# Kernel tuning notes

Measured on AMD Instinct MI355X. Metric: run time of the kernel, lower is better.

Reference implementation:

```python
import jax, jax.numpy as jnp
import numpy as np


def setup_inputs() -> dict:
    key = jax.random.key(0)
    k1, k2, k3 = jax.random.split(key, 3)
    b, n, h, d = 2, 2048, 16, 64
    q = jax.random.normal(k1, (b, n, h, d), dtype=jnp.float32)
    k = jax.random.normal(k2, (b, n, h, d), dtype=jnp.float32)
    v = jax.random.normal(k3, (b, n, h, d), dtype=jnp.float32)
    return {"q": q, "k": k, "v": v, "is_causal": 1}


def reference(q, k, v, is_causal):
    # q, k, v: [b, n, h, d] -> attention computed in [b, h, n, d] layout
    b, n, h, d = q.shape
    scale = 1.0 / jnp.sqrt(jnp.asarray(d, dtype=q.dtype))
    # scores: [b, h, n_q, n_k]
    scores = jnp.einsum("bqhd,bkhd->bhqk", q, k) * scale
    if is_causal:
        causal_mask = jnp.triu(jnp.ones((n, n), dtype=bool), k=1)  # True above diag
        scores = jnp.where(causal_mask[None, None], -jnp.inf, scores)
    attn = jax.nn.softmax(scores, axis=-1)
    out = jnp.einsum("bhqk,bkhd->bqhd", attn, v)  # back to [b, n, h, d]
    return out
```

## Files before the change

kernel.cpp:

```cpp
#include <hip/hip_runtime.h>
#include <hip/hip_bf16.h>

namespace {

constexpr int Nn = 2048;
constexpr int Hh = 16;
constexpr int Dd = 64;
constexpr int ROWSTR = Hh * Dd;
constexpr int KVB = 64;
constexpr int NTILES = Nn / KVB;
constexpr size_t IMG_TILE = 16384;
constexpr size_t WS_NEED = (size_t)32 * NTILES * IMG_TILE;

typedef __bf16 bf16x8 __attribute__((ext_vector_type(8)));
typedef __bf16 bf16x4 __attribute__((ext_vector_type(4)));
typedef float  f32x16 __attribute__((ext_vector_type(16)));

constexpr float MSHIFT = 16.0f;

__device__ __forceinline__ void gload_lds16(const char* g, char* l) {
  __builtin_amdgcn_global_load_lds(
      (const __attribute__((address_space(1))) void*)g,
      (__attribute__((address_space(3))) void*)l, 16, 0, 0);
}
__device__ __forceinline__ void drain_vmcnt0() {
  asm volatile("s_waitcnt vmcnt(0)" ::: "memory");
}

__global__ __launch_bounds__(256, 2) void prep_kernel(
    const float* __restrict__ Kg, const float* __restrict__ Vg,
    char* __restrict__ ws) {
  const int bid = blockIdx.x;
  const int bh  = bid & 31;
  const int T   = bid >> 5;
  const int tid = threadIdx.x;
  const int b = bh >> 4, h = bh & 15;
  const size_t base = ((size_t)b * Nn * Hh + h) * Dd;
  const float* kp = Kg + base;
  const float* vp = Vg + base;
  char* img = ws + (size_t)(bh * NTILES + T) * IMG_TILE;

  {
    const int row = tid >> 2;
    const int seg = tid & 3;
    const float* kr = kp + (size_t)(T * 64 + row) * ROWSTR + seg * 16;
    float4 f0 = ((const float4*)kr)[0];
    float4 f1 = ((const float4*)kr)[1];
    float4 f2 = ((const float4*)kr)[2];
    float4 f3 = ((const float4*)kr)[3];
    const int half = row >> 5, l31r = row & 31;
    char* slotp = img + (half * 4 + seg) * 1024;
    bf16x8 w0 = { (__bf16)f0.x, (__bf16)f0.y, (__bf16)f0.z, (__bf16)f0.w,
                  (__bf16)f1.x, (__bf16)f1.y, (__bf16)f1.z, (__bf16)f1.w };
    bf16x8 w1 = { (__bf16)f2.x, (__bf16)f2.y, (__bf16)f2.z, (__bf16)f2.w,
                  (__bf16)f3.x, (__bf16)f3.y, (__bf16)f3.z, (__bf16)f3.w };
    *(bf16x8*)(slotp + l31r * 16) = w0;
    *(bf16x8*)(slotp + (l31r + 32) * 16) = w1;
  }
  char* imgV = img + 8192;
#pragma unroll
  for (int e2 = 0; e2 < 2; ++e2) {
    const int e = e2 * 256 + tid;
    const int slotV = e >> 6, lane = e & 63;
    const int kc = slotV >> 1, df = slotV & 1;
    const int l31e = lane & 31, g2e = lane >> 5;
    const int d = 32 * df + l31e;
    const size_t kv0 = (size_t)(T * 64 + 16 * kc + 4 * g2e);
    const float* vb = vp + d;
    bf16x8 w;
#pragma unroll
    for (int i2 = 0; i2 < 4; ++i2) w[i2]     = (__bf16)vb[(kv0 + i2) * ROWSTR];
#pragma unroll
    for (int i2 = 0; i2 < 4; ++i2) w[4 + i2] = (__bf16)vb[(kv0 + 8 + i2) * ROWSTR];
    *(bf16x8*)(imgV + slotV * 1024 + lane * 16) = w;
  }
}

__global__ __launch_bounds__(256, 2) void fattn_kernel(
    const float* __restrict__ Qg, const char* __restrict__ ws,
    const int* __restrict__ flag, float* __restrict__ Og) {
  __shared__ __align__(16) char smem[2][2][16384];

  const int tid  = threadIdx.x;
  const int lane = tid & 63;
  const int wv   = tid >> 6;
  const int grp  = wv >> 1;
  const int st   = wv & 1;
  const int l31  = lane & 31;
  const int g2   = lane >> 5;

  const int bid = blockIdx.x;
  const int bh  = ((bid & 7) << 2) | ((bid >> 3) & 3);
  const int j   = bid >> 5;
  const int b   = bh >> 4;
  const int h   = bh & 15;
  const int causal = flag[0];

  const size_t base = ((size_t)b * Nn * Hh + h) * Dd;
  const float* qp = Qg + base;
  const char*  img = ws + (size_t)bh * NTILES * IMG_TILE;
  float*       op = Og + base;

  const float SCALE = 0.125f * 1.44269504088896340736f;

  bf16x8 vone;
#pragma unroll
  for (int e = 0; e < 8; ++e) vone[e] = (__bf16)1.0f;

  for (int pass = 0; pass < 2; ++pass) {
    const int Tq = pass ? j : (31 - j);
    const int qs = Tq * 64 + st * 32;
    const int NI = causal ? ((Tq + 2) >> 1) : (NTILES / 2);
    const int nC = causal ? ((Tq >= grp) ? (((Tq - grp) >> 1) + 1) : 0)
                          : (NTILES / 2);

    __syncthreads();

    bf16x8 qf[4];
#pragma unroll
    for (int dc = 0; dc < 4; ++dc) {
      const float* qrow = qp + (size_t)(qs + l31) * ROWSTR + dc * 16 + g2 * 8;
      float4 a = *(const float4*)qrow;
      float4 c = *(const float4*)(qrow + 4);
      qf[dc][0] = (__bf16)(a.x * SCALE); qf[dc][1] = (__bf16)(a.y * SCALE);
      qf[dc][2] = (__bf16)(a.z * SCALE); qf[dc][3] = (__bf16)(a.w * SCALE);
      qf[dc][4] = (__bf16)(c.x * SCALE); qf[dc][5] = (__bf16)(c.y * SCALE);
      qf[dc][6] = (__bf16)(c.z * SCALE); qf[dc][7] = (__bf16)(c.w * SCALE);
    }

    f32x16 acc0 = {};
    f32x16 acc1 = {};
    f32x16 accl = {};

#pragma unroll
    for (int it = 0; it < 8; ++it)
      gload_lds16(img + (it * 256 + tid) * 16,
                  &smem[0][0][0] + (it * 256 + tid) * 16);
    __builtin_amdgcn_sched_barrier(0);

    for (int i = 0; i < NI; ++i) {
      drain_vmcnt0();
      __syncthreads();
      const bool pf = (i + 1 < NI);
      if (pf) {
        const char* src = img + (size_t)(2 * i + 2) * IMG_TILE;
        char* dst = &smem[(i + 1) & 1][0][0];
#pragma unroll
        for (int it = 0; it < 8; ++it)
          gload_lds16(src + (it * 256 + tid) * 16, dst + (it * 256 + tid) * 16);
        __builtin_amdgcn_sched_barrier(0);
      }

      if (i < nC) {
        const char* kb = &smem[i & 1][grp][0];
        const char* vb = kb + 8192;

        f32x16 s0, s1;
#pragma unroll
        for (int rr = 0; rr < 16; ++rr) { s0[rr] = -MSHIFT; s1[rr] = -MSHIFT; }
        __builtin_amdgcn_s_setprio(1);
#pragma unroll
        for (int dc = 0; dc < 4; ++dc) {
          bf16x8 kf0 = *(const bf16x8*)(kb + (dc)     * 1024 + lane * 16);
          bf16x8 kf1 = *(const bf16x8*)(kb + (4 + dc) * 1024 + lane * 16);
          s0 = __builtin_amdgcn_mfma_f32_32x32x16_bf16(kf0, qf[dc], s0, 0, 0, 0);
          s1 = __builtin_amdgcn_mfma_f32_32x32x16_bf16(kf1, qf[dc], s1, 0, 0, 0);
        }
        __builtin_amdgcn_s_setprio(0);

        if (causal && (2 * i + grp) == Tq) {
          const int kvb = Tq * KVB;
          const int qrow = qs + l31;
#pragma unroll
          for (int rr = 0; rr < 16; ++rr) {
            int rm = (rr & 3) + ((rr >> 2) << 3) + (g2 << 2);
            if (kvb + rm > qrow)      s0[rr] = -INFINITY;
            if (kvb + 32 + rm > qrow) s1[rr] = -INFINITY;
          }
        }

#pragma unroll
        for (int rr = 0; rr < 16; ++rr) {
          s0[rr] = __builtin_amdgcn_exp2f(s0[rr]);
          s1[rr] = __builtin_amdgcn_exp2f(s1[rr]);
        }

        bf16x8 pa[4];
#pragma unroll
        for (int kc = 0; kc < 4; ++kc) {
          const f32x16& sv = (kc < 2) ? s0 : s1;
          const int rbase = (kc & 1) * 8;
#pragma unroll
          for (int jj = 0; jj < 8; ++jj) pa[kc][jj] = (__bf16)sv[rbase + jj];
        }

        __builtin_amdgcn_s_setprio(1);
#pragma unroll
        for (int kc = 0; kc < 4; ++kc) {
          bf16x8 vf0 = *(const bf16x8*)(vb + (kc * 2)     * 1024 + lane * 16);
          bf16x8 vf1 = *(const bf16x8*)(vb + (kc * 2 + 1) * 1024 + lane * 16);
          acc0 = __builtin_amdgcn_mfma_f32_32x32x16_bf16(pa[kc], vf0, acc0, 0, 0, 0);
          acc1 = __builtin_amdgcn_mfma_f32_32x32x16_bf16(pa[kc], vf1, acc1, 0, 0, 0);
          accl = __builtin_amdgcn_mfma_f32_32x32x16_bf16(pa[kc], vone, accl, 0, 0, 0);
        }
        __builtin_amdgcn_s_setprio(0);
      }
    }

    drain_vmcnt0();
    __syncthreads();
    float* arena = (float*)&smem[1][0][0];
    if (grp == 1) {
      float* ab = arena + st * 2112;
#pragma unroll
      for (int rr = 0; rr < 16; ++rr) {
        int rm = (rr & 3) + ((rr >> 2) << 3) + (g2 << 2);
        ab[rm * 64 + l31]      = acc0[rr];
        ab[rm * 64 + 32 + l31] = acc1[rr];
        ab[2048 + rm]          = accl[rr];
      }
    }
    __syncthreads();
    if (grp == 0) {
      const float* ab = arena + st * 2112;
#pragma unroll
      for (int rr = 0; rr < 16; ++rr) {
        const int rm = (rr & 3) + ((rr >> 2) << 3) + (g2 << 2);
        const float lT = accl[rr] + ab[2048 + rm];
        const float li = 1.0f / lT;
        const float o0 = (acc0[rr] + ab[rm * 64 + l31])      * li;
        const float o1 = (acc1[rr] + ab[rm * 64 + 32 + l31]) * li;
        const size_t row = (size_t)(qs + rm) * ROWSTR;
        op[row + l31]      = o0;
        op[row + 32 + l31] = o1;
      }
    }
  }
}

__device__ __forceinline__ int swzK(int row, int colByte) {
  return (row * 128 + colByte) ^ ((row & 7) << 4);
}
__device__ __forceinline__ int swzV(int row, int colByte) {
  return (row * 128 + colByte) ^ (((row & 7) << 4) | (((row >> 3) & 1) << 3));
}
struct SR { float4 k[4]; float v[16]; };
__device__ __forceinline__ void fb_issue(const float* kp, const float* vp,
                                         int kv0, int tid, SR& s) {
#pragma unroll
  for (int it = 0; it < 4; ++it) {
    int idx = it * 256 + tid;
    int kvr = idx >> 4, c4 = idx & 15;
    s.k[it] = *(const float4*)(kp + (size_t)(kv0 + kvr) * ROWSTR + c4 * 4);
  }
#pragma unroll
  for (int it = 0; it < 4; ++it) {
    int idx = it * 256 + tid;
    int d8 = idx & 63, kv4 = idx >> 6;
#pragma unroll
    for (int i2 = 0; i2 < 4; ++i2)
      s.v[it * 4 + i2] = vp[(size_t)(kv0 + kv4 * 4 + i2) * ROWSTR + d8];
  }
}
__device__ __forceinline__ void fb_write(char* kb, char* vb, int tid, const SR& s) {
#pragma unroll
  for (int it = 0; it < 4; ++it) {
    int idx = it * 256 + tid;
    int kvr = idx >> 4, c4 = idx & 15;
    bf16x4 w = { (__bf16)s.k[it].x, (__bf16)s.k[it].y,
                 (__bf16)s.k[it].z, (__bf16)s.k[it].w };
    *(bf16x4*)(kb + swzK(kvr, c4 * 8)) = w;
  }
#pragma unroll
  for (int it = 0; it < 4; ++it) {
    int idx = it * 256 + tid;
    int d8 = idx & 63, kv4 = idx >> 6;
    bf16x4 w = { (__bf16)s.v[it * 4 + 0], (__bf16)s.v[it * 4 + 1],
                 (__bf16)s.v[it * 4 + 2], (__bf16)s.v[it * 4 + 3] };
    *(bf16x4*)(vb + swzV(d8, kv4 * 8)) = w;
  }
}
__global__ __launch_bounds__(256, 2) void fattn_fb(
    const float* __restrict__ Qg, const float* __restrict__ Kg,
    const float* __restrict__ Vg, const int* __restrict__ flag,
    float* __restrict__ Og) {
  __shared__ char smem[16384];
  const int tid  = threadIdx.x;
  const int lane = tid & 63;
  const int wv   = tid >> 6;
  const int l31  = lane & 31;
  const int g2   = lane >> 5;
  const int bid = blockIdx.x;
  const int pidx = bid >> 1;
  const int side = bid & 1;
  const int bh  = ((pidx & 7) << 2) | (pidx >> 6);
  const int ti  = (pidx >> 3) & 7;
  const int b   = bh >> 4;
  const int h   = bh & 15;
  const int causal = flag[0];
  const int Tq  = side ? ti : (15 - ti);
  const size_t base = ((size_t)b * Nn * Hh + h) * Dd;
  const float* qp = Qg + base;
  const float* kp = Kg + base;
  const float* vp = Vg + base;
  float*       op = Og + base;
  const float SCALE = 0.125f * 1.44269504088896340736f;
  const int qs = Tq * 128 + wv * 32;
  const int Tblock = causal ? (2 * Tq + 2) : NTILES;
  const int Twave  = causal ? ((qs + 31) / KVB + 1) : NTILES;
  bf16x8 qf[4];
#pragma unroll
  for (int dc = 0; dc < 4; ++dc) {
    const float* qrow = qp + (size_t)(qs + l31) * ROWSTR + dc * 16 + g2 * 8;
    float4 a = *(const float4*)qrow;
    float4 c = *(const float4*)(qrow + 4);
    qf[dc][0] = (__bf16)(a.x * SCALE); qf[dc][1] = (__bf16)(a.y * SCALE);
    qf[dc][2] = (__bf16)(a.z * SCALE); qf[dc][3] = (__bf16)(a.w * SCALE);
    qf[dc][4] = (__bf16)(c.x * SCALE); qf[dc][5] = (__bf16)(c.y * SCALE);
    qf[dc][6] = (__bf16)(c.z * SCALE); qf[dc][7] = (__bf16)(c.w * SCALE);
  }
  f32x16 acc0 = {}, acc1 = {};
  float m_run = -INFINITY, l_run = 0.0f;
  SR st;
  fb_issue(kp, vp, 0, tid, st);
  fb_write(smem, smem + 8192, tid, st);
  for (int t = 0; t < Tblock; ++t) {
    __syncthreads();
    const bool pf = (t + 1 < Tblock);
    if (pf) fb_issue(kp, vp, (t + 1) * KVB, tid, st);
    if (t < Twave) {
      const char* kb = smem;
      const char* vb = smem + 8192;
      f32x16 s0 = {}, s1 = {};
#pragma unroll
      for (int dc = 0; dc < 4; ++dc) {
        bf16x8 kf0 = *(const bf16x8*)(kb + swzK(l31,      32 * dc + 16 * g2));
        bf16x8 kf1 = *(const bf16x8*)(kb + swzK(32 + l31, 32 * dc + 16 * g2));
        s0 = __builtin_amdgcn_mfma_f32_32x32x16_bf16(kf0, qf[dc], s0, 0, 0, 0);
        s1 = __builtin_amdgcn_mfma_f32_32x32x16_bf16(kf1, qf[dc], s1, 0, 0, 0);
      }
      if (causal && t == Twave - 1) {
        const int kvb = t * KVB;
        const int qrow = qs + l31;
#pragma unroll
        for (int rr = 0; rr < 16; ++rr) {
          int rm = (rr & 3) + ((rr >> 2) << 3) + (g2 << 2);
          if (kvb + rm > qrow)      s0[rr] = -INFINITY;
          if (kvb + 32 + rm > qrow) s1[rr] = -INFINITY;
        }
      }
      float p8[8];
#pragma unroll
      for (int e = 0; e < 8; ++e)
        p8[e] = fmaxf(fmaxf(s0[e], s0[e + 8]), fmaxf(s1[e], s1[e + 8]));
      float mt = fmaxf(fmaxf(fmaxf(p8[0], p8[1]), fmaxf(p8[2], p8[3])),
                       fmaxf(fmaxf(p8[4], p8[5]), fmaxf(p8[6], p8[7])));
      mt = fmaxf(mt, __shfl_xor(mt, 32));
      const float mnew = fmaxf(m_run, mt);
#pragma unroll
      for (int rr = 0; rr < 16; ++rr) {
        s0[rr] = __builtin_amdgcn_exp2f(s0[rr] - mnew);
        s1[rr] = __builtin_amdgcn_exp2f(s1[rr] - mnew);
      }
      float q8[8];
#pragma unroll
      for (int e = 0; e < 8; ++e)
        q8[e] = (s0[e] + s0[e + 8]) + (s1[e] + s1[e + 8]);
      float rs = ((q8[0] + q8[1]) + (q8[2] + q8[3])) +
                 ((q8[4] + q8[5]) + (q8[6] + q8[7]));
      rs += __shfl_xor(rs, 32);
      if (__all(mt <= m_run)) {
        l_run += rs;
      } else {
        const float alpha = __builtin_amdgcn_exp2f(m_run - mnew);
#pragma unroll
        for (int rr = 0; rr < 16; ++rr) {
          float at = __shfl(alpha, (rr & 3) + ((rr >> 2) << 3) + (g2 << 2));
          acc0[rr] *= at;
          acc1[rr] *= at;
        }
        l_run = l_run * alpha + rs;
        m_run = mnew;
      }
      bf16x8 pa[4];
#pragma unroll
      for (int kc = 0; kc < 4; ++kc) {
        const f32x16& sv = (kc < 2) ? s0 : s1;
        const int rbase = (kc & 1) * 8;
#pragma unroll
        for (int jj = 0; jj < 8; ++jj) pa[kc][jj] = (__bf16)sv[rbase + jj];
      }
#pragma unroll
      for (int kc = 0; kc < 4; ++kc) {
        const int cb = 32 * kc + 8 * g2;
#pragma unroll
        for (int df = 0; df < 2; ++df) {
          const int row = 32 * df + l31;
          bf16x4 v0 = *(const bf16x4*)(vb + swzV(row, cb));
          bf16x4 v1 = *(const bf16x4*)(vb + swzV(row, cb + 16));
          bf16x8 vf = __builtin_shufflevector(v0, v1, 0, 1, 2, 3, 4, 5, 6, 7);
          if (df == 0)
            acc0 = __builtin_amdgcn_mfma_f32_32x32x16_bf16(pa[kc], vf, acc0, 0, 0, 0);
          else
            acc1 = __builtin_amdgcn_mfma_f32_32x32x16_bf16(pa[kc], vf, acc1, 0, 0, 0);
        }
      }
    }
    __syncthreads();
    if (pf) fb_write(smem, smem + 8192, tid, st);
  }
  const float linv = 1.0f / l_run;
#pragma unroll
  for (int rr = 0; rr < 16; ++rr) {
    const int rm = (rr & 3) + ((rr >> 2) << 3) + (g2 << 2);
    const float li = __shfl(linv, rm);
    const size_t row = (size_t)(qs + rm) * ROWSTR;
    op[row + l31]      = acc0[rr] * li;
    op[row + 32 + l31] = acc1[rr] * li;
  }
}

}

extern "C" void kernel_launch(void* const* d_in, const int* in_sizes, int n_in,
                              void* d_out, int out_size, void* d_ws, size_t ws_size,
                              hipStream_t stream) {
  (void)in_sizes; (void)n_in; (void)out_size;
  const float* q = (const float*)d_in[0];
  const float* k = (const float*)d_in[1];
  const float* v = (const float*)d_in[2];
  const int* flag = (const int*)d_in[3];
  float* out = (float*)d_out;
  if (ws_size >= WS_NEED) {
    char* ws = (char*)d_ws;
    prep_kernel<<<dim3(1024), dim3(256), 0, stream>>>(k, v, ws);
    fattn_kernel<<<dim3(512), dim3(256), 0, stream>>>(q, ws, flag, out);
  } else {
    fattn_fb<<<dim3(512), dim3(256), 0, stream>>>(q, k, v, flag, out);
  }
}
```

Baseline: 44.57 us.

## Split attention into 32-row query tiles with 4-way per-wave KV split

Query tiles shrink from 64 to 32 rows and each of the four waves now takes every fourth 32-key KV tile with its own double-buffered LDS region. Each wave runs its own pipeline with no block-wide barrier per iteration, and the grid doubles to 1024 blocks. At the end, three waves' partial results are reduced through LDS into wave 0. The aim is finer causal load balance, more parallelism and no per-tile syncs, at the cost of more Q reloads, a larger cross-wave reduction, and fewer MFMAs per loaded tile.

```diff
diff --git a/kernel.cpp b/kernel.cpp
--- a/kernel.cpp
+++ b/kernel.cpp
@@ -7,10 +7,10 @@
 constexpr int Hh = 16;
 constexpr int Dd = 64;
 constexpr int ROWSTR = Hh * Dd;
-constexpr int KVB = 64;
-constexpr int NTILES = Nn / KVB;
-constexpr size_t IMG_TILE = 16384;
-constexpr size_t WS_NEED = (size_t)32 * NTILES * IMG_TILE;
+constexpr int KVB = 32;
+constexpr int NT32 = Nn / KVB;
+constexpr size_t IMG_TILE = 8192;
+constexpr size_t WS_NEED = (size_t)32 * NT32 * IMG_TILE;
 
 typedef __bf16 bf16x8 __attribute__((ext_vector_type(8)));
 typedef __bf16 bf16x4 __attribute__((ext_vector_type(4)));
@@ -32,24 +32,24 @@
     char* __restrict__ ws) {
   const int bid = blockIdx.x;
   const int bh  = bid & 31;
-  const int T   = bid >> 5;
+  const int m   = bid >> 5;
   const int tid = threadIdx.x;
   const int b = bh >> 4, h = bh & 15;
   const size_t base = ((size_t)b * Nn * Hh + h) * Dd;
   const float* kp = Kg + base;
   const float* vp = Vg + base;
-  char* img = ws + (size_t)(bh * NTILES + T) * IMG_TILE;
+  char* img0 = ws + (size_t)(bh * NT32 + 2 * m) * IMG_TILE;
 
   {
     const int row = tid >> 2;
     const int seg = tid & 3;
-    const float* kr = kp + (size_t)(T * 64 + row) * ROWSTR + seg * 16;
+    const float* kr = kp + (size_t)(m * 64 + row) * ROWSTR + seg * 16;
     float4 f0 = ((const float4*)kr)[0];
     float4 f1 = ((const float4*)kr)[1];
     float4 f2 = ((const float4*)kr)[2];
     float4 f3 = ((const float4*)kr)[3];
-    const int half = row >> 5, l31r = row & 31;
-    char* slotp = img + (half * 4 + seg) * 1024;
+    char* slotp = img0 + (row >> 5) * IMG_TILE + seg * 1024;
+    const int l31r = row & 31;
     bf16x8 w0 = { (__bf16)f0.x, (__bf16)f0.y, (__bf16)f0.z, (__bf16)f0.w,
                   (__bf16)f1.x, (__bf16)f1.y, (__bf16)f1.z, (__bf16)f1.w };
     bf16x8 w1 = { (__bf16)f2.x, (__bf16)f2.y, (__bf16)f2.z, (__bf16)f2.w,
@@ -57,35 +57,35 @@
     *(bf16x8*)(slotp + l31r * 16) = w0;
     *(bf16x8*)(slotp + (l31r + 32) * 16) = w1;
   }
-  char* imgV = img + 8192;
 #pragma unroll
   for (int e2 = 0; e2 < 2; ++e2) {
     const int e = e2 * 256 + tid;
-    const int slotV = e >> 6, lane = e & 63;
-    const int kc = slotV >> 1, df = slotV & 1;
+    const int im = e >> 8;
+    const int r  = e & 255;
+    const int slotV = r >> 6;
+    const int lane  = r & 63;
+    const int kc2 = slotV >> 1, df = slotV & 1;
     const int l31e = lane & 31, g2e = lane >> 5;
     const int d = 32 * df + l31e;
-    const size_t kv0 = (size_t)(T * 64 + 16 * kc + 4 * g2e);
+    const size_t kv0 = (size_t)(m * 64 + im * 32 + 16 * kc2 + 4 * g2e);
     const float* vb = vp + d;
     bf16x8 w;
 #pragma unroll
     for (int i2 = 0; i2 < 4; ++i2) w[i2]     = (__bf16)vb[(kv0 + i2) * ROWSTR];
 #pragma unroll
     for (int i2 = 0; i2 < 4; ++i2) w[4 + i2] = (__bf16)vb[(kv0 + 8 + i2) * ROWSTR];
-    *(bf16x8*)(imgV + slotV * 1024 + lane * 16) = w;
+    *(bf16x8*)(img0 + im * IMG_TILE + 4096 + slotV * 1024 + lane * 16) = w;
   }
 }
 
 __global__ __launch_bounds__(256, 2) void fattn_kernel(
     const float* __restrict__ Qg, const char* __restrict__ ws,
     const int* __restrict__ flag, float* __restrict__ Og) {
-  __shared__ __align__(16) char smem[2][2][16384];
+  __shared__ __align__(16) char smem[4][2][8192];
 
   const int tid  = threadIdx.x;
   const int lane = tid & 63;
   const int wv   = tid >> 6;
-  const int grp  = wv >> 1;
-  const int st   = wv & 1;
   const int l31  = lane & 31;
   const int g2   = lane >> 5;
 
@@ -98,7 +98,7 @@
 
   const size_t base = ((size_t)b * Nn * Hh + h) * Dd;
   const float* qp = Qg + base;
-  const char*  img = ws + (size_t)bh * NTILES * IMG_TILE;
+  const char*  img = ws + (size_t)bh * NT32 * IMG_TILE;
   float*       op = Og + base;
 
   const float SCALE = 0.125f * 1.44269504088896340736f;
@@ -107,12 +107,14 @@
 #pragma unroll
   for (int e = 0; e < 8; ++e) vone[e] = (__bf16)1.0f;
 
+  char* buf0 = &smem[wv][0][0];
+  char* buf1 = &smem[wv][1][0];
+
   for (int pass = 0; pass < 2; ++pass) {
-    const int Tq = pass ? j : (31 - j);
-    const int qs = Tq * 64 + st * 32;
-    const int NI = causal ? ((Tq + 2) >> 1) : (NTILES / 2);
-    const int nC = causal ? ((Tq >= grp) ? (((Tq - grp) >> 1) + 1) : 0)
-                          : (NTILES / 2);
+    const int Tq = pass ? j : (63 - j);
+    const int qs = Tq * 32;
+    const int TL = causal ? Tq : (NT32 - 1);
+    const int nC = (TL >= wv) ? (((TL - wv) >> 2) + 1) : 0;
 
     __syncthreads();
 
@@ -132,86 +134,75 @@
     f32x16 acc1 = {};
     f32x16 accl = {};
 
-#pragma unroll
-    for (int it = 0; it < 8; ++it)
-      gload_lds16(img + (it * 256 + tid) * 16,
-                  &smem[0][0][0] + (it * 256 + tid) * 16);
-    __builtin_amdgcn_sched_barrier(0);
-
-    for (int i = 0; i < NI; ++i) {
+    if (nC > 0) {
+      const char* src = img + (size_t)wv * IMG_TILE;
+#pragma unroll
+      for (int it = 0; it < 8; ++it)
+        gload_lds16(src + it * 1024 + lane * 16, buf0 + it * 1024 + lane * 16);
+    }
+
+    for (int i = 0; i < nC; ++i) {
+      const int t = wv + 4 * i;
       drain_vmcnt0();
-      __syncthreads();
-      const bool pf = (i + 1 < NI);
-      if (pf) {
-        const char* src = img + (size_t)(2 * i + 2) * IMG_TILE;
-        char* dst = &smem[(i + 1) & 1][0][0];
+      __builtin_amdgcn_sched_barrier(0);
+      if (i + 1 < nC) {
+        const char* src = img + (size_t)(t + 4) * IMG_TILE;
+        char* dst = (i & 1) ? buf0 : buf1;
 #pragma unroll
         for (int it = 0; it < 8; ++it)
-          gload_lds16(src + (it * 256 + tid) * 16, dst + (it * 256 + tid) * 16);
+          gload_lds16(src + it * 1024 + lane * 16, dst + it * 1024 + lane * 16);
         __builtin_amdgcn_sched_barrier(0);
       }
-
-      if (i < nC) {
-        const char* kb = &smem[i & 1][grp][0];
-        const char* vb = kb + 8192;
-
-        f32x16 s0, s1;
-#pragma unroll
-        for (int rr = 0; rr < 16; ++rr) { s0[rr] = -MSHIFT; s1[rr] = -MSHIFT; }
-        __builtin_amdgcn_s_setprio(1);
-#pragma unroll
-        for (int dc = 0; dc < 4; ++dc) {
-          bf16x8 kf0 = *(const bf16x8*)(kb + (dc)     * 1024 + lane * 16);
-          bf16x8 kf1 = *(const bf16x8*)(kb + (4 + dc) * 1024 + lane * 16);
-          s0 = __builtin_amdgcn_mfma_f32_32x32x16_bf16(kf0, qf[dc], s0, 0, 0, 0);
-          s1 = __builtin_amdgcn_mfma_f32_32x32x16_bf16(kf1, qf[dc], s1, 0, 0, 0);
+      const char* kb = (i & 1) ? buf1 : buf0;
+      const char* vb = kb + 4096;
+
+      f32x16 s0;
+#pragma unroll
+      for (int rr = 0; rr < 16; ++rr) s0[rr] = -MSHIFT;
+      __builtin_amdgcn_s_setprio(1);
+#pragma unroll
+      for (int dc = 0; dc < 4; ++dc) {
+        bf16x8 kf = *(const bf16x8*)(kb + dc * 1024 + lane * 16);
+        s0 = __builtin_amdgcn_mfma_f32_32x32x16_bf16(kf, qf[dc], s0, 0, 0, 0);
+      }
+      __builtin_amdgcn_s_setprio(0);
+
+      if (causal && t == TL) {
+        const int kvb = t * KVB;
+        const int qrow = qs + l31;
+#pragma unroll
+        for (int rr = 0; rr < 16; ++rr) {
+          int rm = (rr & 3) + ((rr >> 2) << 3) + (g2 << 2);
+          if (kvb + rm > qrow) s0[rr] = -INFINITY;
         }
-        __builtin_amdgcn_s_setprio(0);
-
-        if (causal && (2 * i + grp) == Tq) {
-          const int kvb = Tq * KVB;
-          const int qrow = qs + l31;
-#pragma unroll
-          for (int rr = 0; rr < 16; ++rr) {
-            int rm = (rr & 3) + ((rr >> 2) << 3) + (g2 << 2);
-            if (kvb + rm > qrow)      s0[rr] = -INFINITY;
-            if (kvb + 32 + rm > qrow) s1[rr] = -INFINITY;
-          }
-        }
-
-#pragma unroll
-        for (int rr = 0; rr < 16; ++rr) {
-          s0[rr] = __builtin_amdgcn_exp2f(s0[rr]);
-          s1[rr] = __builtin_amdgcn_exp2f(s1[rr]);
-        }
-
-        bf16x8 pa[4];
-#pragma unroll
-        for (int kc = 0; kc < 4; ++kc) {
-          const f32x16& sv = (kc < 2) ? s0 : s1;
-          const int rbase = (kc & 1) * 8;
-#pragma unroll
-          for (int jj = 0; jj < 8; ++jj) pa[kc][jj] = (__bf16)sv[rbase + jj];
-        }
-
-        __builtin_amdgcn_s_setprio(1);
-#pragma unroll
-        for (int kc = 0; kc < 4; ++kc) {
-          bf16x8 vf0 = *(const bf16x8*)(vb + (kc * 2)     * 1024 + lane * 16);
-          bf16x8 vf1 = *(const bf16x8*)(vb + (kc * 2 + 1) * 1024 + lane * 16);
-          acc0 = __builtin_amdgcn_mfma_f32_32x32x16_bf16(pa[kc], vf0, acc0, 0, 0, 0);
-          acc1 = __builtin_amdgcn_mfma_f32_32x32x16_bf16(pa[kc], vf1, acc1, 0, 0, 0);
-          accl = __builtin_amdgcn_mfma_f32_32x32x16_bf16(pa[kc], vone, accl, 0, 0, 0);
-        }
-        __builtin_amdgcn_s_setprio(0);
-      }
-    }
-
-    drain_vmcnt0();
-    __syncthreads();
-    float* arena = (float*)&smem[1][0][0];
-    if (grp == 1) {
-      float* ab = arena + st * 2112;
+      }
+
+#pragma unroll
+      for (int rr = 0; rr < 16; ++rr) s0[rr] = __builtin_amdgcn_exp2f(s0[rr]);
+
+      bf16x8 pa0, pa1;
+#pragma unroll
+      for (int jj = 0; jj < 8; ++jj) { pa0[jj] = (__bf16)s0[jj];
+                                       pa1[jj] = (__bf16)s0[8 + jj]; }
+
+      __builtin_amdgcn_s_setprio(1);
+      {
+        bf16x8 v00 = *(const bf16x8*)(vb + 0 * 1024 + lane * 16);
+        bf16x8 v01 = *(const bf16x8*)(vb + 1 * 1024 + lane * 16);
+        bf16x8 v10 = *(const bf16x8*)(vb + 2 * 1024 + lane * 16);
+        bf16x8 v11 = *(const bf16x8*)(vb + 3 * 1024 + lane * 16);
+        acc0 = __builtin_amdgcn_mfma_f32_32x32x16_bf16(pa0, v00, acc0, 0, 0, 0);
+        acc1 = __builtin_amdgcn_mfma_f32_32x32x16_bf16(pa0, v01, acc1, 0, 0, 0);
+        accl = __builtin_amdgcn_mfma_f32_32x32x16_bf16(pa0, vone, accl, 0, 0, 0);
+        acc0 = __builtin_amdgcn_mfma_f32_32x32x16_bf16(pa1, v10, acc0, 0, 0, 0);
+        acc1 = __builtin_amdgcn_mfma_f32_32x32x16_bf16(pa1, v11, acc1, 0, 0, 0);
+        accl = __builtin_amdgcn_mfma_f32_32x32x16_bf16(pa1, vone, accl, 0, 0, 0);
+      }
+      __builtin_amdgcn_s_setprio(0);
+    }
+
+    if (wv != 0) {
+      float* ab = (float*)&smem[wv][0][0];
 #pragma unroll
       for (int rr = 0; rr < 16; ++rr) {
         int rm = (rr & 3) + ((rr >> 2) << 3) + (g2 << 2);
@@ -221,15 +212,19 @@
       }
     }
     __syncthreads();
-    if (grp == 0) {
-      const float* ab = arena + st * 2112;
+    if (wv == 0) {
+      const float* a1 = (const float*)&smem[1][0][0];
+      const float* a2 = (const float*)&smem[2][0][0];
+      const float* a3 = (const float*)&smem[3][0][0];
 #pragma unroll
       for (int rr = 0; rr < 16; ++rr) {
         const int rm = (rr & 3) + ((rr >> 2) << 3) + (g2 << 2);
-        const float lT = accl[rr] + ab[2048 + rm];
+        const float lT = accl[rr] + a1[2048 + rm] + a2[2048 + rm] + a3[2048 + rm];
         const float li = 1.0f / lT;
-        const float o0 = (acc0[rr] + ab[rm * 64 + l31])      * li;
-        const float o1 = (acc1[rr] + ab[rm * 64 + 32 + l31]) * li;
+        const float o0 = (acc0[rr] + a1[rm * 64 + l31] +
+                          a2[rm * 64 + l31] + a3[rm * 64 + l31]) * li;
+        const float o1 = (acc1[rr] + a1[rm * 64 + 32 + l31] +
+                          a2[rm * 64 + 32 + l31] + a3[rm * 64 + 32 + l31]) * li;
         const size_t row = (size_t)(qs + rm) * ROWSTR;
         op[row + l31]      = o0;
         op[row + 32 + l31] = o1;
@@ -306,8 +301,8 @@
   float*       op = Og + base;
   const float SCALE = 0.125f * 1.44269504088896340736f;
   const int qs = Tq * 128 + wv * 32;
-  const int Tblock = causal ? (2 * Tq + 2) : NTILES;
-  const int Twave  = causal ? ((qs + 31) / KVB + 1) : NTILES;
+  const int Tblock = causal ? (2 * Tq + 2) : 32;
+  const int Twave  = causal ? ((qs + 31) / 64 + 1) : 32;
   bf16x8 qf[4];
 #pragma unroll
   for (int dc = 0; dc < 4; ++dc) {
@@ -327,7 +322,7 @@
   for (int t = 0; t < Tblock; ++t) {
     __syncthreads();
     const bool pf = (t + 1 < Tblock);
-    if (pf) fb_issue(kp, vp, (t + 1) * KVB, tid, st);
+    if (pf) fb_issue(kp, vp, (t + 1) * 64, tid, st);
     if (t < Twave) {
       const char* kb = smem;
       const char* vb = smem + 8192;
@@ -340,7 +335,7 @@
         s1 = __builtin_amdgcn_mfma_f32_32x32x16_bf16(kf1, qf[dc], s1, 0, 0, 0);
       }
       if (causal && t == Twave - 1) {
-        const int kvb = t * KVB;
+        const int kvb = t * 64;
         const int qrow = qs + l31;
 #pragma unroll
         for (int rr = 0; rr < 16; ++rr) {
@@ -434,7 +429,7 @@
   if (ws_size >= WS_NEED) {
     char* ws = (char*)d_ws;
     prep_kernel<<<dim3(1024), dim3(256), 0, stream>>>(k, v, ws);
-    fattn_kernel<<<dim3(512), dim3(256), 0, stream>>>(q, ws, flag, out);
+    fattn_kernel<<<dim3(1024), dim3(256), 0, stream>>>(q, ws, flag, out);
   } else {
     fattn_fb<<<dim3(512), dim3(256), 0, stream>>>(q, k, v, flag, out);
   }
```

Result: slower. 57.36 us (+28.7%).
